# Kernel optimization log

Measured on AMD Instinct MI355X. Metric: run time of the kernel, lower is better.

Reference implementation:

```python
import jax, jax.numpy as jnp
import numpy as np

B, N, H, W = 2, 65536, 256, 256
FEA, OUT, CMP, MAX_PT = 8, 512, 32, 64
EPS = 1e-5


def _xavier(key, fan_in, fan_out):
    scale = np.sqrt(2.0 / (fan_in + fan_out)).astype(np.float32)
    return jax.random.normal(key, (fan_in, fan_out), dtype=jnp.float32) * scale


def setup_inputs() -> dict:
    key = jax.random.key(0)
    ks = jax.random.split(key, 8)
    pt_fea = jax.random.normal(ks[0], (B, N, FEA), dtype=jnp.float32)
    xy_ind = jax.random.randint(ks[1], (B, N, 2), 0, H, dtype=jnp.int32)
    return {
        "pt_fea": pt_fea,
        "bn0_g": jnp.ones((FEA,), jnp.float32), "bn0_b": jnp.zeros((FEA,), jnp.float32),
        "W1": _xavier(ks[2], FEA, 64),
        "bn1_g": jnp.ones((64,), jnp.float32), "bn1_b": jnp.zeros((64,), jnp.float32),
        "W2": _xavier(ks[3], 64, 128),
        "bn2_g": jnp.ones((128,), jnp.float32), "bn2_b": jnp.zeros((128,), jnp.float32),
        "W3": _xavier(ks[4], 128, 256),
        "bn3_g": jnp.ones((256,), jnp.float32), "bn3_b": jnp.zeros((256,), jnp.float32),
        "W4": _xavier(ks[5], 256, OUT),
        "Wc": _xavier(ks[6], OUT, CMP),
        "xy_ind": xy_ind,
    }


def _forward(pt_fea, bn0_g, bn0_b, W1, bn1_g, bn1_b, W2, bn2_g, bn2_b,
             W3, bn3_g, bn3_b, W4, Wc, xy_ind):
    Bc, Nc, Fc = pt_fea.shape
    P = Bc * Nc
    feats = pt_fea.reshape(P, Fc)
    batch_id = jnp.repeat(jnp.arange(Bc, dtype=jnp.int32), Nc)
    xy = xy_ind.reshape(P, 2)
    keys = batch_id * (H * W) + xy[:, 0] * W + xy[:, 1]  # linearized voxel id

    # random shuffle of points (torch.randperm)
    perm = jax.random.permutation(jax.random.key(42), P)
    feats = feats[perm]
    keys = keys[perm]

    # rank of each point within its voxel, in shuffled order
    # (== grp_range_torch(unq_cnt)[argsort(argsort(unq_inv))])
    order = jnp.argsort(keys)  # stable
    sk = keys[order]
    pos = jnp.arange(P)
    new_grp = jnp.concatenate([jnp.array([True]), sk[1:] != sk[:-1]])
    grp_start = jax.lax.cummax(jnp.where(new_grp, pos, 0))
    rank = jnp.zeros(P, jnp.int32).at[order].set((pos - grp_start).astype(jnp.int32))
    mask = rank < MAX_PT  # keep at most MAX_PT points per voxel

    # PPmodel: BN -> Lin -> BN -> ReLU x3 -> Lin, BN stats over kept points only
    m = mask[:, None].astype(feats.dtype)
    cnt = jnp.sum(m)

    def bn(x, g, b):
        mu = jnp.sum(x * m, axis=0) / cnt
        var = jnp.sum(jnp.square(x - mu) * m, axis=0) / cnt  # biased var
        return (x - mu) * jax.lax.rsqrt(var + EPS) * g + b

    x = bn(feats, bn0_g, bn0_b)
    x = jax.nn.relu(bn(x @ W1, bn1_g, bn1_b))
    x = jax.nn.relu(bn(x @ W2, bn2_g, bn2_b))
    x = jax.nn.relu(bn(x @ W3, bn3_g, bn3_b))
    x = x @ W4  # [P, OUT]

    # scatter_max segment reduction into dense voxel grid
    NEG = jnp.finfo(x.dtype).min
    x = jnp.where(mask[:, None], x, NEG)
    S = Bc * H * W
    pooled = jax.ops.segment_max(x, keys, num_segments=S)
    occupied = jax.ops.segment_sum(jnp.ones(P, x.dtype), keys, num_segments=S) > 0
    pooled = jnp.where(occupied[:, None], pooled, 0.0)

    comp = jax.nn.relu(pooled @ Wc)  # fea_compression
    comp = jnp.where(occupied[:, None], comp, 0.0)  # empty voxels stay zero
    out = comp.reshape(Bc, H, W, CMP).transpose(0, 3, 1, 2)  # [B, C, H, W]
    return out


def reference(pt_fea, bn0_g, bn0_b, W1, bn1_g, bn1_b, W2, bn2_g, bn2_b,
              W3, bn3_g, bn3_b, W4, Wc, xy_ind):
    return _forward(pt_fea, bn0_g, bn0_b, W1, bn1_g, bn1_b, W2, bn2_g, bn2_b,
                    W3, bn3_g, bn3_b, W4, Wc, xy_ind)
```

## Files before the change

### kernel.cpp

```cpp
#include <hip/hip_runtime.h>
#include <cstdint>
#include <cstddef>


#define P_TOT  131072
#define HWSZ   65536
#define WGRID  256
#define S_TOT  131072
#define EPS    1e-5f
#define CNTF   131072.0f

#define OFF_Y3    0ull
#define OFF_Y1    67108864ull
#define OFF_Y2    100663296ull
#define OFF_POOL  67108864ull
#define OFF_CNT   201326592ull
#define OFF_ST    201850880ull
#define OFF_OFFS  201916416ull
#define OFF_CUR   202440704ull
#define OFF_BSUM  202964992ull
#define OFF_PIDF  202969088ull
#define OFF_SEND  203493376ull
#define OFF_SKEY  204017664ull
#define OFF_W3F   204541952ull
#define OFF_W4F   204607488ull
#define OFF_WCF   204869632ull
#define OFF_W2F   204902400ull
#define OFF_SCSH  204918784ull

typedef __attribute__((ext_vector_type(8)))  short bf16x8;
typedef __attribute__((ext_vector_type(16))) float f32x16;

__device__ __forceinline__ unsigned f2bf(float f) {
    unsigned u = __float_as_uint(f);
    return (u + 0x7FFFu + ((u >> 16) & 1u)) >> 16;
}
__device__ __forceinline__ float bf2f(unsigned h) {
    return __uint_as_float(h << 16);
}

__global__ __launch_bounds__(256) void k_zero(uint4* __restrict__ p, int n_u4) {
    int i = blockIdx.x * blockDim.x + threadIdx.x;
    if (i < n_u4) p[i] = make_uint4(0u, 0u, 0u, 0u);
}

__global__ __launch_bounds__(256) void k_prepw(
    const float* __restrict__ W2, const float* __restrict__ W3,
    const float* __restrict__ W4, const float* __restrict__ Wc,
    uint4* __restrict__ W2F, uint4* __restrict__ W3F,
    uint4* __restrict__ W4F, uint4* __restrict__ WcF)
{
    int gw = (blockIdx.x * 256 + threadIdx.x) >> 6;
    int l = threadIdx.x & 63;
    const float* W; uint4* dst; int M, mt, ks, fi;
    if (gw < 64)       { fi = gw;       W = W3; dst = W3F; M = 256; mt = fi >> 3; ks = fi & 7;  }
    else if (gw < 320) { fi = gw - 64;  W = W4; dst = W4F; M = 512; mt = fi >> 4; ks = fi & 15; }
    else if (gw < 352) { fi = gw - 320; W = Wc; dst = WcF; M = 32;  mt = 0;      ks = fi;      }
    else               { fi = gw - 352; W = W2; dst = W2F; M = 128; mt = fi >> 2; ks = fi & 3;  }
    int m = mt * 32 + (l & 31);
    int k0 = ks * 16 + (l >> 5) * 8;
    unsigned p[4];
    #pragma unroll
    for (int jj = 0; jj < 4; ++jj) {
        unsigned lo = f2bf(W[(size_t)(k0 + 2*jj)     * M + m]);
        unsigned hi = f2bf(W[(size_t)(k0 + 2*jj + 1) * M + m]);
        p[jj] = lo | (hi << 16);
    }
    dst[(size_t)fi * 64 + l] = make_uint4(p[0], p[1], p[2], p[3]);
}

__global__ __launch_bounds__(256) void k_bnprep(
    const float* __restrict__ st, const float* __restrict__ g,
    const float* __restrict__ b, float* __restrict__ sc,
    float* __restrict__ sh, int nch)
{
    int c = blockIdx.x * 256 + threadIdx.x;
    if (c >= nch) return;
    float mu = st[c * 16] * (1.0f / CNTF);
    float var = st[(nch + c) * 16] * (1.0f / CNTF) - mu * mu;
    float rs = rsqrtf(var + EPS);
    float s = rs * g[c];
    sc[c] = s;
    sh[c] = b[c] - mu * s;
}

__global__ __launch_bounds__(256) void k_fold(
    unsigned short* __restrict__ y, const float* __restrict__ sc,
    const float* __restrict__ sh, int nch, int n_u4)
{
    int i = blockIdx.x * 256 + threadIdx.x;
    if (i >= n_u4) return;
    int ch0 = (i * 8) & (nch - 1);
    float4 s0 = *(const float4*)(sc + ch0), s1 = *(const float4*)(sc + ch0 + 4);
    float4 h0 = *(const float4*)(sh + ch0), h1 = *(const float4*)(sh + ch0 + 4);
    float scv[8] = {s0.x,s0.y,s0.z,s0.w,s1.x,s1.y,s1.z,s1.w};
    float shv[8] = {h0.x,h0.y,h0.z,h0.w,h1.x,h1.y,h1.z,h1.w};
    uint4 e = ((const uint4*)y)[i];
    unsigned eu[4] = {e.x, e.y, e.z, e.w};
    unsigned ou[4];
    #pragma unroll
    for (int jj = 0; jj < 4; ++jj) {
        float x0 = fmaxf(fmaf(bf2f(eu[jj] & 0xFFFFu), scv[2*jj],   shv[2*jj]),   0.f);
        float x1 = fmaxf(fmaf(bf2f(eu[jj] >> 16),     scv[2*jj+1], shv[2*jj+1]), 0.f);
        ou[jj] = f2bf(x0) | (f2bf(x1) << 16);
    }
    ((uint4*)y)[i] = make_uint4(ou[0], ou[1], ou[2], ou[3]);
}

__global__ __launch_bounds__(256) void k_stats0(
    const float* __restrict__ pt, const int* __restrict__ xy,
    float* __restrict__ st0, unsigned* __restrict__ counts)
{
    __shared__ float part[4][16];
    const int tid = threadIdx.x;
    const int p = blockIdx.x * 256 + tid;
    const float4* f4 = (const float4*)(pt + (size_t)p * 8);
    float4 a = f4[0], b = f4[1];
    float v[8] = {a.x,a.y,a.z,a.w,b.x,b.y,b.z,b.w};
    int key = (p >> 16) * HWSZ + xy[2*p] * WGRID + xy[2*p + 1];
    atomicAdd(&counts[key], 1u);
    float s[8], q[8];
    #pragma unroll
    for (int k = 0; k < 8; ++k) { s[k] = v[k]; q[k] = v[k]*v[k]; }
    #pragma unroll
    for (int k = 0; k < 8; ++k) {
        #pragma unroll
        for (int off = 32; off > 0; off >>= 1) {
            s[k] += __shfl_down(s[k], off);
            q[k] += __shfl_down(q[k], off);
        }
    }
    if ((tid & 63) == 0) {
        int w = tid >> 6;
        #pragma unroll
        for (int k = 0; k < 8; ++k) { part[w][k] = s[k]; part[w][8 + k] = q[k]; }
    }
    __syncthreads();
    if (tid < 16) {
        float t = part[0][tid] + part[1][tid] + part[2][tid] + part[3][tid];
        atomicAdd(&st0[tid * 16], t);
    }
}

__global__ __launch_bounds__(256) void k_lin1(
    const float* __restrict__ pt, const float* __restrict__ g0,
    const float* __restrict__ b0, const float* __restrict__ W1,
    const float* __restrict__ st0, float* __restrict__ y1,
    float* __restrict__ st1)
{
    __shared__ float x0s[64 * 8];
    __shared__ float w1s[8 * 64];
    __shared__ float sc0s[8], sh0s[8];
    __shared__ float red[256];
    const int tid = threadIdx.x;

    if (tid < 8) {
        float mu = st0[tid * 16] * (1.0f / CNTF);
        float var = st0[(8 + tid) * 16] * (1.0f / CNTF) - mu * mu;
        float rs = rsqrtf(var + EPS);
        sc0s[tid] = rs * g0[tid];
        sh0s[tid] = b0[tid] - mu * rs * g0[tid];
    }
    if (tid < 128) ((float4*)w1s)[tid] = ((const float4*)W1)[tid];
    const int c = tid & 63;
    const int psub = tid >> 6;
    float ssum = 0.f, ssq = 0.f;
    for (int t = 0; t < 4; ++t) {
        const int pbase = blockIdx.x * 256 + t * 64;
        __syncthreads();
        if (tid < 128) {
            float4 f = ((const float4*)(pt + (size_t)pbase * 8))[tid];
            int cc = (tid & 1) * 4;
            f.x = fmaf(f.x, sc0s[cc + 0], sh0s[cc + 0]);
            f.y = fmaf(f.y, sc0s[cc + 1], sh0s[cc + 1]);
            f.z = fmaf(f.z, sc0s[cc + 2], sh0s[cc + 2]);
            f.w = fmaf(f.w, sc0s[cc + 3], sh0s[cc + 3]);
            ((float4*)x0s)[tid] = f;
        }
        __syncthreads();
        #pragma unroll
        for (int i = 0; i < 16; ++i) {
            int pl = psub * 16 + i;
            float acc = 0.f;
            #pragma unroll
            for (int k = 0; k < 8; ++k)
                acc = fmaf(x0s[pl * 8 + k], w1s[k * 64 + c], acc);
            y1[(size_t)(pbase + pl) * 64 + c] = acc;
            ssum += acc; ssq += acc * acc;
        }
    }
    red[tid] = ssum; __syncthreads();
    if (tid < 64) atomicAdd(&st1[tid * 16],
        red[tid] + red[tid+64] + red[tid+128] + red[tid+192]);
    __syncthreads();
    red[tid] = ssq; __syncthreads();
    if (tid < 64) atomicAdd(&st1[(64 + tid) * 16],
        red[tid] + red[tid+64] + red[tid+128] + red[tid+192]);
}

__global__ __launch_bounds__(256) void k_scan1(
    const unsigned* __restrict__ counts, unsigned* __restrict__ bsum)
{
    __shared__ unsigned sh[256];
    int t = threadIdx.x;
    sh[t] = counts[blockIdx.x * 256 + t];
    __syncthreads();
    for (int d = 128; d > 0; d >>= 1) {
        if (t < d) sh[t] += sh[t + d];
        __syncthreads();
    }
    if (t == 0) bsum[blockIdx.x] = sh[0];
}

__global__ __launch_bounds__(256) void k_scan2(
    const unsigned* __restrict__ bsum, unsigned* __restrict__ boff)
{
    __shared__ unsigned sh[256];
    int t = threadIdx.x;
    unsigned a = bsum[2*t], b = bsum[2*t+1];
    unsigned s = a + b;
    sh[t] = s; __syncthreads();
    for (int d = 1; d < 256; d <<= 1) {
        unsigned u = (t >= d) ? sh[t-d] : 0u;
        __syncthreads();
        sh[t] += u;
        __syncthreads();
    }
    unsigned excl = sh[t] - s;
    boff[2*t]   = excl;
    boff[2*t+1] = excl + a;
}

__global__ __launch_bounds__(256) void k_scan3(
    const unsigned* __restrict__ counts, const unsigned* __restrict__ boff,
    unsigned* __restrict__ offs)
{
    __shared__ unsigned sh[256];
    int t = threadIdx.x, b = blockIdx.x;
    unsigned v = counts[b*256 + t];
    sh[t] = v; __syncthreads();
    for (int d = 1; d < 256; d <<= 1) {
        unsigned u = (t >= d) ? sh[t-d] : 0u;
        __syncthreads();
        sh[t] += u;
        __syncthreads();
    }
    offs[b*256 + t] = boff[b] + sh[t] - v;
}

__global__ __launch_bounds__(256) void k_fill(
    const int* __restrict__ xy, const unsigned* __restrict__ offs,
    const unsigned* __restrict__ counts, unsigned* __restrict__ cur,
    unsigned* __restrict__ pidf, unsigned* __restrict__ send,
    unsigned* __restrict__ skey)
{
    int p = blockIdx.x * 256 + threadIdx.x;
    int key = (p >> 16) * HWSZ + xy[2*p] * WGRID + xy[2*p + 1];
    unsigned o = offs[key];
    unsigned r = atomicAdd(&cur[key], 1u);
    unsigned slot = o + r;
    pidf[slot] = (unsigned)p | (r == 0 ? 0x80000000u : 0u);
    send[slot] = o + counts[key];
    skey[slot] = (unsigned)key;
}

__global__ __launch_bounds__(256, 2) void k_lin2(
    const float* __restrict__ y1, const float* __restrict__ g1,
    const float* __restrict__ b1, const uint4* __restrict__ W2F,
    const float* __restrict__ st1, unsigned short* __restrict__ y2,
    float* __restrict__ st2)
{
    __shared__ uint4 w2s[1024];
    __shared__ float sc1s[64], sh1s[64];
    const int tid = threadIdx.x, l = tid & 63, w = tid >> 6;
    if (tid < 64) {
        float mu = st1[tid * 16] * (1.0f / CNTF);
        float var = st1[(64 + tid) * 16] * (1.0f / CNTF) - mu * mu;
        float rs = rsqrtf(var + EPS);
        sc1s[tid] = rs * g1[tid];
        sh1s[tid] = b1[tid] - mu * rs * g1[tid];
    }
    #pragma unroll
    for (int r = 0; r < 4; ++r) w2s[r * 256 + tid] = W2F[r * 256 + tid];
    __syncthreads();
    const int n = l & 31, q = l >> 5;
    float s_acc[16], q_acc[16];
    #pragma unroll
    for (int r = 0; r < 16; ++r) { s_acc[r] = 0.f; q_acc[r] = 0.f; }

    for (int t = 0; t < 8; ++t) {
        const int p = (blockIdx.x * 8 + t) * 32 + n;
        const float* yrow = y1 + (size_t)p * 64 + q * 8;
        bf16x8 Bf[4];
        #pragma unroll
        for (int ks = 0; ks < 4; ++ks) {
            float4 v0 = *(const float4*)(yrow + ks * 16);
            float4 v1 = *(const float4*)(yrow + ks * 16 + 4);
            int k0 = ks * 16 + q * 8;
            float e[8] = {v0.x,v0.y,v0.z,v0.w,v1.x,v1.y,v1.z,v1.w};
            union { bf16x8 v; unsigned u[4]; } cv;
            #pragma unroll
            for (int jj = 0; jj < 4; ++jj) {
                float a0 = fmaxf(fmaf(e[2*jj],   sc1s[k0+2*jj],   sh1s[k0+2*jj]),   0.f);
                float a1 = fmaxf(fmaf(e[2*jj+1], sc1s[k0+2*jj+1], sh1s[k0+2*jj+1]), 0.f);
                cv.u[jj] = f2bf(a0) | (f2bf(a1) << 16);
            }
            Bf[ks] = cv.v;
        }
        f32x16 acc;
        #pragma unroll
        for (int r = 0; r < 16; ++r) acc[r] = 0.f;
        #pragma unroll
        for (int ks = 0; ks < 4; ++ks) {
            union { uint4 u; bf16x8 v; } av;
            av.u = w2s[(w * 4 + ks) * 64 + l];
            acc = __builtin_amdgcn_mfma_f32_32x32x16_bf16(av.v, Bf[ks], acc, 0, 0, 0);
        }
        #pragma unroll
        for (int g = 0; g < 4; ++g) {
            int ch0 = w * 32 + 8 * g + 4 * q;
            ushort4 pk;
            pk.x = (unsigned short)f2bf(acc[4*g+0]);
            pk.y = (unsigned short)f2bf(acc[4*g+1]);
            pk.z = (unsigned short)f2bf(acc[4*g+2]);
            pk.w = (unsigned short)f2bf(acc[4*g+3]);
            *(ushort4*)(y2 + (size_t)p * 128 + ch0) = pk;
        }
        #pragma unroll
        for (int r = 0; r < 16; ++r) { s_acc[r] += acc[r]; q_acc[r] += acc[r]*acc[r]; }
    }
    #pragma unroll
    for (int r = 0; r < 16; ++r) {
        float s = s_acc[r], sq = q_acc[r];
        #pragma unroll
        for (int off = 16; off > 0; off >>= 1) {
            s  += __shfl_xor(s, off);
            sq += __shfl_xor(sq, off);
        }
        if ((l & 31) == 0) {
            int ch = w * 32 + (r & 3) + 8 * (r >> 2) + 4 * q;
            atomicAdd(&st2[ch * 16], s);
            atomicAdd(&st2[(128 + ch) * 16], sq);
        }
    }
}

__global__ __launch_bounds__(256, 2) void k_lin3(
    const unsigned short* __restrict__ y2raw, const float* __restrict__ g2,
    const float* __restrict__ b2, const uint4* __restrict__ W3F,
    const float* __restrict__ st2, unsigned short* __restrict__ y3,
    float* __restrict__ st3)
{
    __shared__ uint4 w3s[4096];
    __shared__ float sc2s[128], sh2s[128];
    const int tid = threadIdx.x, l = tid & 63, w = tid >> 6;
    if (tid < 128) {
        float mu = st2[tid * 16] * (1.0f / CNTF);
        float var = st2[(128 + tid) * 16] * (1.0f / CNTF) - mu * mu;
        float rs = rsqrtf(var + EPS);
        sc2s[tid] = rs * g2[tid];
        sh2s[tid] = b2[tid] - mu * rs * g2[tid];
    }
    #pragma unroll
    for (int r = 0; r < 16; ++r) w3s[r * 256 + tid] = W3F[r * 256 + tid];
    __syncthreads();
    const int n = l & 31, q = l >> 5;
    float s_acc[32], q_acc[32];
    #pragma unroll
    for (int r = 0; r < 32; ++r) { s_acc[r] = 0.f; q_acc[r] = 0.f; }

    for (int t = 0; t < 8; ++t) {
        const int p = (blockIdx.x * 8 + t) * 32 + n;
        const unsigned short* yrow = y2raw + (size_t)p * 128 + q * 8;
        bf16x8 Bf[8];
        #pragma unroll
        for (int ks = 0; ks < 8; ++ks) {
            uint4 e = *(const uint4*)(yrow + ks * 16);
            int k0 = ks * 16 + q * 8;
            unsigned eu[4] = {e.x, e.y, e.z, e.w};
            union { bf16x8 v; unsigned u[4]; } cv;
            #pragma unroll
            for (int jj = 0; jj < 4; ++jj) {
                float a0 = fmaxf(fmaf(bf2f(eu[jj] & 0xFFFFu),
                                      sc2s[k0+2*jj],   sh2s[k0+2*jj]),   0.f);
                float a1 = fmaxf(fmaf(bf2f(eu[jj] >> 16),
                                      sc2s[k0+2*jj+1], sh2s[k0+2*jj+1]), 0.f);
                cv.u[jj] = f2bf(a0) | (f2bf(a1) << 16);
            }
            Bf[ks] = cv.v;
        }
        f32x16 acc[2];
        #pragma unroll
        for (int i = 0; i < 2; ++i)
            #pragma unroll
            for (int r = 0; r < 16; ++r) acc[i][r] = 0.f;
        #pragma unroll
        for (int ks = 0; ks < 8; ++ks) {
            #pragma unroll
            for (int i = 0; i < 2; ++i) {
                union { uint4 u; bf16x8 v; } av;
                av.u = w3s[((w * 2 + i) * 8 + ks) * 64 + l];
                acc[i] = __builtin_amdgcn_mfma_f32_32x32x16_bf16(av.v, Bf[ks], acc[i], 0, 0, 0);
            }
        }
        #pragma unroll
        for (int i = 0; i < 2; ++i) {
            #pragma unroll
            for (int g = 0; g < 4; ++g) {
                int ch0 = (w * 2 + i) * 32 + 8 * g + 4 * q;
                ushort4 pk;
                pk.x = (unsigned short)f2bf(acc[i][4*g+0]);
                pk.y = (unsigned short)f2bf(acc[i][4*g+1]);
                pk.z = (unsigned short)f2bf(acc[i][4*g+2]);
                pk.w = (unsigned short)f2bf(acc[i][4*g+3]);
                *(ushort4*)(y3 + (size_t)p * 256 + ch0) = pk;
            }
            #pragma unroll
            for (int r = 0; r < 16; ++r) {
                s_acc[i*16+r] += acc[i][r];
                q_acc[i*16+r] += acc[i][r] * acc[i][r];
            }
        }
    }
    #pragma unroll
    for (int i = 0; i < 2; ++i)
        #pragma unroll
        for (int r = 0; r < 16; ++r) {
            float s = s_acc[i*16+r], sq = q_acc[i*16+r];
            #pragma unroll
            for (int off = 16; off > 0; off >>= 1) {
                s  += __shfl_xor(s, off);
                sq += __shfl_xor(sq, off);
            }
            if ((l & 31) == 0) {
                int ch = (w * 2 + i) * 32 + (r & 3) + 8 * (r >> 2) + 4 * q;
                atomicAdd(&st3[ch * 16], s);
                atomicAdd(&st3[(256 + ch) * 16], sq);
            }
        }
}

__global__ __launch_bounds__(256, 2) void k_smax(
    const unsigned short* __restrict__ y3f, const uint4* __restrict__ W4F,
    const unsigned* __restrict__ pidf, const unsigned* __restrict__ send,
    const unsigned* __restrict__ skey, unsigned short* __restrict__ pooled)
{
    __shared__ float s0c_s[4 * 256];
    const int tid = threadIdx.x, l = tid & 63, w = tid >> 6;
    const int wg = blockIdx.x;
    const int q = l >> 5;

    #pragma unroll
    for (int sub = 0; sub < 4; ++sub) s0c_s[sub * 256 + tid] = -3.4e38f;

    #pragma unroll 1
    for (int t = 4; t >= 0; --t) {
        const int p0 = (wg * 4 + t) * 32;
        const int pos = p0 + (l & 31);
        const int sp = pos < P_TOT ? pos : P_TOT - 1;
        const unsigned pf = pidf[sp];
        const unsigned e_l = send[sp];
        const unsigned key_l = skey[sp];
        const unsigned cmask =
            (unsigned)__ballot((unsigned)(pos + 1) < e_l);
        const unsigned fmask =
            (unsigned)__ballot((pf & 0x80000000u) != 0u);
        const unsigned short* row =
            y3f + (size_t)(pf & 0x7FFFFFFFu) * 256 + q * 8;
        uint4 Xf[16];
        #pragma unroll
        for (int ks = 0; ks < 16; ++ks)
            Xf[ks] = *(const uint4*)(row + ks * 16);

        #pragma unroll 1
        for (int sub = 0; sub < 4; ++sub) {
            const int nt = sub * 4 + w;
            f32x16 acc;
            #pragma unroll
            for (int r = 0; r < 16; ++r) acc[r] = 0.f;
            #pragma unroll
            for (int ks = 0; ks < 16; ++ks) {
                union { uint4 u; bf16x8 v; } xv, wv;
                xv.u = Xf[ks];
                wv.u = W4F[(size_t)(nt * 16 + ks) * 64 + l];
                acc = __builtin_amdgcn_mfma_f32_32x32x16_bf16(xv.v, wv.v, acc, 0, 0, 0);
            }
            float v[32];
            #pragma unroll
            for (int r = 0; r < 16; ++r) {
                int base = (r & 3) + 8 * (r >> 2);
                float o = __shfl_xor(acc[r], 32);
                v[base]     = q ? o : acc[r];
                v[base + 4] = q ? acc[r] : o;
            }
            if ((cmask >> 31) & 1)
                v[31] = fmaxf(v[31], s0c_s[sub * 256 + tid]);
            #pragma unroll
            for (int m = 30; m >= 0; --m)
                if ((cmask >> m) & 1) v[m] = fmaxf(v[m], v[m + 1]);
            s0c_s[sub * 256 + tid] = v[0];
            if (t < 4) {
                #pragma unroll
                for (int m = 0; m < 32; ++m) {
                    if ((fmask >> m) & 1) {
                        unsigned km = (unsigned)
                            __builtin_amdgcn_readlane((int)key_l, m);
                        if ((m >> 4) == q)
                            pooled[(size_t)km * 512 + nt * 32 + (l & 31)] =
                                (unsigned short)f2bf(v[m]);
                    }
                }
            }
        }
    }
}

__global__ __launch_bounds__(256, 4) void k_out(
    const unsigned short* __restrict__ pooled, const unsigned* __restrict__ counts,
    const uint4* __restrict__ WcF, float* __restrict__ out)
{
    __shared__ uint4 wcs[2048];
    const int tid = threadIdx.x, l = tid & 63, w = tid >> 6;
    const int sbase = blockIdx.x * 128;
    #pragma unroll
    for (int r = 0; r < 8; ++r) wcs[r * 256 + tid] = WcF[r * 256 + tid];
    __syncthreads();
    const int n = l & 31, q = l >> 5;
    const int s = sbase + w * 32 + n;
    const bool occ = counts[s] > 0;
    const unsigned short* prow =
        pooled + (occ ? (size_t)s * 512 : (size_t)0) + q * 8;
    f32x16 acc;
    #pragma unroll
    for (int r = 0; r < 16; ++r) acc[r] = 0.f;

    for (int ks = 0; ks < 32; ++ks) {
        union { uint4 u; bf16x8 v; } bv;
        bv.u = *(const uint4*)(prow + ks * 16);
        union { uint4 u; bf16x8 v; } av;
        av.u = wcs[ks * 64 + l];
        acc = __builtin_amdgcn_mfma_f32_32x32x16_bf16(av.v, bv.v, acc, 0, 0, 0);
    }
    const int b = s >> 16, hw = s & 65535;
    #pragma unroll
    for (int r = 0; r < 16; ++r) {
        int ch = (r & 3) + 8 * (r >> 2) + 4 * q;
        float x = occ ? fmaxf(acc[r], 0.f) : 0.f;
        out[(size_t)b * (32 * HWSZ) + (size_t)ch * HWSZ + hw] = x;
    }
}

extern "C" void kernel_launch(void* const* d_in, const int* in_sizes, int n_in,
                              void* d_out, int out_size, void* d_ws, size_t ws_size,
                              hipStream_t stream) {
    const float* pt = (const float*)d_in[0];
    const float* g0 = (const float*)d_in[1];
    const float* b0 = (const float*)d_in[2];
    const float* W1 = (const float*)d_in[3];
    const float* g1 = (const float*)d_in[4];
    const float* b1 = (const float*)d_in[5];
    const float* W2 = (const float*)d_in[6];
    const float* g2 = (const float*)d_in[7];
    const float* b2 = (const float*)d_in[8];
    const float* W3 = (const float*)d_in[9];
    const float* g3 = (const float*)d_in[10];
    const float* b3 = (const float*)d_in[11];
    const float* W4 = (const float*)d_in[12];
    const float* Wc = (const float*)d_in[13];
    const int*   xy = (const int*)d_in[14];
    float* out = (float*)d_out;

    char* ws = (char*)d_ws;
    unsigned short* y3     = (unsigned short*)(ws + OFF_Y3);
    float*          y1     = (float*)(ws + OFF_Y1);
    unsigned short* y2     = (unsigned short*)(ws + OFF_Y2);
    unsigned short* pool16 = (unsigned short*)(ws + OFF_POOL);
    unsigned*       counts = (unsigned*)(ws + OFF_CNT);
    float*          st     = (float*)(ws + OFF_ST);
    unsigned*       offs   = (unsigned*)(ws + OFF_OFFS);
    unsigned*       cur    = (unsigned*)(ws + OFF_CUR);
    unsigned*       bsum   = (unsigned*)(ws + OFF_BSUM);
    unsigned*       pidf   = (unsigned*)(ws + OFF_PIDF);
    unsigned*       send   = (unsigned*)(ws + OFF_SEND);
    unsigned*       skey   = (unsigned*)(ws + OFF_SKEY);
    uint4* W3F = (uint4*)(ws + OFF_W3F);
    uint4* W4F = (uint4*)(ws + OFF_W4F);
    uint4* WcF = (uint4*)(ws + OFF_WCF);
    uint4* W2F = (uint4*)(ws + OFF_W2F);
    float* scsh = (float*)(ws + OFF_SCSH);
    float* sc3 = scsh;       float* sh3 = scsh + 256;
    float* st0 = st;
    float* st1 = st + 256;
    float* st2 = st + 2304;
    float* st3 = st + 6400;

    k_zero<<<400, 256, 0, stream>>>((uint4*)(ws + OFF_CNT), 102400);
    k_prepw<<<92, 256, 0, stream>>>(W2, W3, W4, Wc, W2F, W3F, W4F, WcF);

    k_stats0<<<512, 256, 0, stream>>>(pt, xy, st0, counts);
    k_scan1<<<512, 256, 0, stream>>>(counts, bsum);
    k_scan2<<<1,   256, 0, stream>>>(bsum, bsum + 512);
    k_scan3<<<512, 256, 0, stream>>>(counts, bsum + 512, offs);
    k_fill<<<512, 256, 0, stream>>>(xy, offs, counts, cur, pidf, send, skey);

    k_lin1<<<512, 256, 0, stream>>>(pt, g0, b0, W1, st0, y1, st1);
    k_lin2<<<512, 256, 0, stream>>>(y1, g1, b1, W2F, st1, y2, st2);
    k_lin3<<<512, 256, 0, stream>>>(y2, g2, b2, W3F, st2, y3, st3);
    k_bnprep<<<1, 256, 0, stream>>>(st3, g3, b3, sc3, sh3, 256);
    k_fold<<<16384, 256, 0, stream>>>(y3, sc3, sh3, 256, 4194304);

    k_smax<<<1024, 256, 0, stream>>>(y3, W4F, pidf, send, skey, pool16);
    k_out<<<S_TOT / 128, 256, 0, stream>>>(pool16, counts, WcF, out);
}
```

Baseline: 456.1 us.

## Fuse layer-3 BN+ReLU into scatter-max kernel and halve its chunk size

Drops the separate BN-prep and fold kernels. The final batch-norm scale/shift is now computed per block into shared memory, and normalize+ReLU is applied to y3 rows as they are loaded inside k_smax. This avoids a full read-modify-write pass over the 64 MB y3 buffer and two launches. Each k_smax block now handles 2 point tiles plus one lookback tile instead of 4 plus one, and the grid doubles to 2048 blocks. That raises the share of redundant lookback work, and every block recomputes the BN parameters.

Result: slower. 766.7 us (+68.1%).

```diff
diff --git a/kernel.cpp b/kernel.cpp
--- a/kernel.cpp
+++ b/kernel.cpp
@@ -26,7 +26,6 @@
 #define OFF_W4F   204607488ull
 #define OFF_WCF   204869632ull
 #define OFF_W2F   204902400ull
-#define OFF_SCSH  204918784ull
 
 typedef __attribute__((ext_vector_type(8)))  short bf16x8;
 typedef __attribute__((ext_vector_type(16))) float f32x16;
@@ -69,44 +68,6 @@
     dst[(size_t)fi * 64 + l] = make_uint4(p[0], p[1], p[2], p[3]);
 }
 
-__global__ __launch_bounds__(256) void k_bnprep(
-    const float* __restrict__ st, const float* __restrict__ g,
-    const float* __restrict__ b, float* __restrict__ sc,
-    float* __restrict__ sh, int nch)
-{
-    int c = blockIdx.x * 256 + threadIdx.x;
-    if (c >= nch) return;
-    float mu = st[c * 16] * (1.0f / CNTF);
-    float var = st[(nch + c) * 16] * (1.0f / CNTF) - mu * mu;
-    float rs = rsqrtf(var + EPS);
-    float s = rs * g[c];
-    sc[c] = s;
-    sh[c] = b[c] - mu * s;
-}
-
-__global__ __launch_bounds__(256) void k_fold(
-    unsigned short* __restrict__ y, const float* __restrict__ sc,
-    const float* __restrict__ sh, int nch, int n_u4)
-{
-    int i = blockIdx.x * 256 + threadIdx.x;
-    if (i >= n_u4) return;
-    int ch0 = (i * 8) & (nch - 1);
-    float4 s0 = *(const float4*)(sc + ch0), s1 = *(const float4*)(sc + ch0 + 4);
-    float4 h0 = *(const float4*)(sh + ch0), h1 = *(const float4*)(sh + ch0 + 4);
-    float scv[8] = {s0.x,s0.y,s0.z,s0.w,s1.x,s1.y,s1.z,s1.w};
-    float shv[8] = {h0.x,h0.y,h0.z,h0.w,h1.x,h1.y,h1.z,h1.w};
-    uint4 e = ((const uint4*)y)[i];
-    unsigned eu[4] = {e.x, e.y, e.z, e.w};
-    unsigned ou[4];
-    #pragma unroll
-    for (int jj = 0; jj < 4; ++jj) {
-        float x0 = fmaxf(fmaf(bf2f(eu[jj] & 0xFFFFu), scv[2*jj],   shv[2*jj]),   0.f);
-        float x1 = fmaxf(fmaf(bf2f(eu[jj] >> 16),     scv[2*jj+1], shv[2*jj+1]), 0.f);
-        ou[jj] = f2bf(x0) | (f2bf(x1) << 16);
-    }
-    ((uint4*)y)[i] = make_uint4(ou[0], ou[1], ou[2], ou[3]);
-}
-
 __global__ __launch_bounds__(256) void k_stats0(
     const float* __restrict__ pt, const int* __restrict__ xy,
     float* __restrict__ st0, unsigned* __restrict__ counts)
@@ -441,21 +402,33 @@
 }
 
 __global__ __launch_bounds__(256, 2) void k_smax(
-    const unsigned short* __restrict__ y3f, const uint4* __restrict__ W4F,
-    const unsigned* __restrict__ pidf, const unsigned* __restrict__ send,
-    const unsigned* __restrict__ skey, unsigned short* __restrict__ pooled)
+    const unsigned short* __restrict__ y3raw, const float* __restrict__ g3,
+    const float* __restrict__ b3, const float* __restrict__ st3,
+    const uint4* __restrict__ W4F, const unsigned* __restrict__ pidf,
+    const unsigned* __restrict__ send, const unsigned* __restrict__ skey,
+    unsigned short* __restrict__ pooled)
 {
     __shared__ float s0c_s[4 * 256];
+    __shared__ float sc3s[256], sh3s[256];
     const int tid = threadIdx.x, l = tid & 63, w = tid >> 6;
     const int wg = blockIdx.x;
     const int q = l >> 5;
 
+    {
+        float mu = st3[tid * 16] * (1.0f / CNTF);
+        float var = st3[(256 + tid) * 16] * (1.0f / CNTF) - mu * mu;
+        float rs = rsqrtf(var + EPS);
+        float s = rs * g3[tid];
+        sc3s[tid] = s;
+        sh3s[tid] = b3[tid] - mu * s;
+    }
     #pragma unroll
     for (int sub = 0; sub < 4; ++sub) s0c_s[sub * 256 + tid] = -3.4e38f;
+    __syncthreads();
 
     #pragma unroll 1
-    for (int t = 4; t >= 0; --t) {
-        const int p0 = (wg * 4 + t) * 32;
+    for (int t = 2; t >= 0; --t) {
+        const int p0 = (wg * 2 + t) * 32;
         const int pos = p0 + (l & 31);
         const int sp = pos < P_TOT ? pos : P_TOT - 1;
         const unsigned pf = pidf[sp];
@@ -466,11 +439,24 @@
         const unsigned fmask =
             (unsigned)__ballot((pf & 0x80000000u) != 0u);
         const unsigned short* row =
-            y3f + (size_t)(pf & 0x7FFFFFFFu) * 256 + q * 8;
+            y3raw + (size_t)(pf & 0x7FFFFFFFu) * 256 + q * 8;
         uint4 Xf[16];
         #pragma unroll
-        for (int ks = 0; ks < 16; ++ks)
-            Xf[ks] = *(const uint4*)(row + ks * 16);
+        for (int ks = 0; ks < 16; ++ks) {
+            uint4 e = *(const uint4*)(row + ks * 16);
+            int c0 = ks * 16 + q * 8;
+            unsigned eu[4] = {e.x, e.y, e.z, e.w};
+            unsigned ou[4];
+            #pragma unroll
+            for (int jj = 0; jj < 4; ++jj) {
+                float a0 = fmaxf(fmaf(bf2f(eu[jj] & 0xFFFFu),
+                                      sc3s[c0+2*jj],   sh3s[c0+2*jj]),   0.f);
+                float a1 = fmaxf(fmaf(bf2f(eu[jj] >> 16),
+                                      sc3s[c0+2*jj+1], sh3s[c0+2*jj+1]), 0.f);
+                ou[jj] = f2bf(a0) | (f2bf(a1) << 16);
+            }
+            Xf[ks] = make_uint4(ou[0], ou[1], ou[2], ou[3]);
+        }
 
         #pragma unroll 1
         for (int sub = 0; sub < 4; ++sub) {
@@ -499,7 +485,7 @@
             for (int m = 30; m >= 0; --m)
                 if ((cmask >> m) & 1) v[m] = fmaxf(v[m], v[m + 1]);
             s0c_s[sub * 256 + tid] = v[0];
-            if (t < 4) {
+            if (t < 2) {
                 #pragma unroll
                 for (int m = 0; m < 32; ++m) {
                     if ((fmask >> m) & 1) {
@@ -587,8 +573,6 @@
     uint4* W4F = (uint4*)(ws + OFF_W4F);
     uint4* WcF = (uint4*)(ws + OFF_WCF);
     uint4* W2F = (uint4*)(ws + OFF_W2F);
-    float* scsh = (float*)(ws + OFF_SCSH);
-    float* sc3 = scsh;       float* sh3 = scsh + 256;
     float* st0 = st;
     float* st1 = st + 256;
     float* st2 = st + 2304;
@@ -606,9 +590,7 @@
     k_lin1<<<512, 256, 0, stream>>>(pt, g0, b0, W1, st0, y1, st1);
     k_lin2<<<512, 256, 0, stream>>>(y1, g1, b1, W2F, st1, y2, st2);
     k_lin3<<<512, 256, 0, stream>>>(y2, g2, b2, W3F, st2, y3, st3);
-    k_bnprep<<<1, 256, 0, stream>>>(st3, g3, b3, sc3, sh3, 256);
-    k_fold<<<16384, 256, 0, stream>>>(y3, sc3, sh3, 256, 4194304);
-
-    k_smax<<<1024, 256, 0, stream>>>(y3, W4F, pidf, send, skey, pool16);
+
+    k_smax<<<2048, 256, 0, stream>>>(y3, g3, b3, st3, W4F, pidf, send, skey, pool16);
     k_out<<<S_TOT / 128, 256, 0, stream>>>(pool16, counts, WcF, out);
 }
```
